# Performance work log

Hardware: AMD Instinct MI355X
Metric: run time of the kernel (lower is better)

## Reference

```python
import jax, jax.numpy as jnp
import numpy as np

N = 100000   # nodes
E = 1600000  # edges per meta-path graph
D_IN = 256
H = 4        # num_heads
F = 32       # out_feats per head
D_HID = H * F  # 128
D_SEM = 128  # semantic attention hidden dim
C = 8        # output classes
NEG_SLOPE = 0.2


def setup_inputs() -> dict:
    key = jax.random.key(0)
    ks = jax.random.split(key, 24)
    inp = {
        "x": jax.random.normal(ks[0], (N, D_IN), dtype=jnp.float32),
        "src0": jax.random.randint(ks[1], (E,), 0, N),
        "dst0": jax.random.randint(ks[2], (E,), 0, N),
        "ew0": jax.random.uniform(ks[3], (E,), dtype=jnp.float32),
        "src1": jax.random.randint(ks[4], (E,), 0, N),
        "dst1": jax.random.randint(ks[5], (E,), 0, N),
        "ew1": jax.random.uniform(ks[6], (E,), dtype=jnp.float32),
    }
    s_in = 1.0 / np.sqrt(D_IN)
    s_f = 1.0 / np.sqrt(F)
    s_h = 1.0 / np.sqrt(D_HID)
    s_s = 1.0 / np.sqrt(D_SEM)
    # GAT params for meta-path 0 and 1 (tuple feat -> separate fc_src/fc_dst)
    inp["Wsrc0"] = jax.random.normal(ks[7], (D_IN, D_HID), dtype=jnp.float32) * s_in
    inp["Wdst0"] = jax.random.normal(ks[8], (D_IN, D_HID), dtype=jnp.float32) * s_in
    inp["al0"] = jax.random.normal(ks[9], (H, F), dtype=jnp.float32) * s_f
    inp["ar0"] = jax.random.normal(ks[10], (H, F), dtype=jnp.float32) * s_f
    inp["b0"] = jnp.zeros((D_HID,), dtype=jnp.float32)
    inp["Wsrc1"] = jax.random.normal(ks[11], (D_IN, D_HID), dtype=jnp.float32) * s_in
    inp["Wdst1"] = jax.random.normal(ks[12], (D_IN, D_HID), dtype=jnp.float32) * s_in
    inp["al1"] = jax.random.normal(ks[13], (H, F), dtype=jnp.float32) * s_f
    inp["ar1"] = jax.random.normal(ks[14], (H, F), dtype=jnp.float32) * s_f
    inp["b1"] = jnp.zeros((D_HID,), dtype=jnp.float32)
    # Semantic attention: Linear(D_HID->128) -> tanh -> Linear(128->1, no bias)
    inp["Wp1"] = jax.random.normal(ks[15], (D_HID, D_SEM), dtype=jnp.float32) * s_h
    inp["bp1"] = jnp.zeros((D_SEM,), dtype=jnp.float32)
    inp["Wp2"] = jax.random.normal(ks[16], (D_SEM, 1), dtype=jnp.float32) * s_s
    # Prediction head
    inp["Wo"] = jax.random.normal(ks[17], (D_HID, C), dtype=jnp.float32) * s_h
    inp["bo"] = jnp.zeros((C,), dtype=jnp.float32)
    return inp


def gat_conv(x, Wsrc, Wdst, al, ar, b, src, dst, ew):
    # feat_src/feat_dst: [N, H, F]
    fs = (x @ Wsrc).reshape(N, H, F)
    fd = (x @ Wdst).reshape(N, H, F)
    el = jnp.einsum('nhf,hf->nh', fs, al)  # [N, H]
    er = jnp.einsum('nhf,hf->nh', fd, ar)  # [N, H]
    e = jax.nn.leaky_relu(el[src] + er[dst], negative_slope=NEG_SLOPE)  # [E, H]
    a = jax.nn.sigmoid(e) * ew[:, None]  # [E, H]  (sigmoid attention * edge_weight)
    m = fs[src] * a[:, :, None]  # [E, H, F]
    out = jax.ops.segment_sum(m, dst, num_segments=N)  # [N, H, F]
    out = out + b.reshape(1, H, F)
    return jax.nn.elu(out).reshape(N, H * F)


def semantic_attention(z, Wp1, bp1, Wp2):
    # z: [N, P, D_HID]
    w = jnp.tanh(z @ Wp1 + bp1) @ Wp2  # [N, P, 1]
    w = w.mean(axis=0)                  # [P, 1]
    beta = jax.nn.softmax(w, axis=0)    # softmax over meta-paths
    return (beta[None] * z).sum(axis=1)  # [N, D_HID]


def reference(x, src0, dst0, ew0, src1, dst1, ew1,
              Wsrc0, Wdst0, al0, ar0, b0,
              Wsrc1, Wdst1, al1, ar1, b1,
              Wp1, bp1, Wp2, Wo, bo):
    z0 = gat_conv(x, Wsrc0, Wdst0, al0, ar0, b0, src0, dst0, ew0)
    z1 = gat_conv(x, Wsrc1, Wdst1, al1, ar1, b1, src1, dst1, ew1)
    z = jnp.stack([z0, z1], axis=1)  # [N, 2, H*F]
    h = semantic_attention(z, Wp1, bp1, Wp2)  # [N, H*F]
    return h @ Wo + bo  # [N, C]
```

## Files before the change

kernel.cpp:

```cpp
#include <hip/hip_runtime.h>
#include <hip/hip_fp16.h>
#include <math.h>

#define N_NODES 100000
#define N_EDGES 1600000
#define D_IN    256
#define D_HID   128
#define NH      4
#define NF      32
#define D_SEM   128
#define NC      8
#define NEG_SLOPE 0.2f
#define BUCKET  64
#define BIN_SHIFT 9
#define BINS    196
#define BIN_CAP 9216
#define CHUNK   8192

typedef _Float16 half8 __attribute__((ext_vector_type(8)));
typedef float    floatx4 __attribute__((ext_vector_type(4)));

struct BinArgs {
    const int*   src[2];
    const int*   dst[2];
    const float* ew[2];
    int*         gcur[2];
    uint2*       binned[2];
};
struct BucketArgs {
    const int*   gcur[2];
    const uint2* binned[2];
    int*         cnt[2];
    unsigned*    edg[2];
};

__global__ __launch_bounds__(256) void prep(const float* __restrict__ Ws0,
                                            const float* __restrict__ Ws1,
                                            const float* __restrict__ Wd0,
                                            const float* __restrict__ ar0,
                                            const float* __restrict__ Wd1,
                                            const float* __restrict__ ar1,
                                            const float* __restrict__ Wp1,
                                            __half* __restrict__ WTA,
                                            __half* __restrict__ WP1T) {
    int g = blockIdx.x * 256 + threadIdx.x;
    if (g < 32768) {
        int col = g >> 8, k = g & 255;
        WTA[(size_t)col*256 + k] = __float2half_rn(Ws0[k*D_HID + col]);
    } else if (g < 65536) {
        int g2 = g - 32768;
        int col = g2 >> 8, k = g2 & 255;
        WTA[(size_t)(128 + col)*256 + k] = __float2half_rn(Ws1[k*D_HID + col]);
    } else if (g < 69632) {
        int g2 = g - 65536;
        int j = g2 >> 8, k = g2 & 255;
        float s = 0.f;
        if (j < 8) {
            int p = j >> 2, h = j & 3;
            const float* Wd = p ? Wd1 : Wd0;
            const float* ar = p ? ar1 : ar0;
            for (int f = 0; f < NF; ++f)
                s = fmaf(Wd[k*D_HID + h*NF + f], ar[h*NF + f], s);
        }
        WTA[(size_t)(256 + j)*256 + k] = __float2half_rn(s);
    } else if (g < 86016) {
        int g2 = g - 69632;
        int c = g2 >> 7, k = g2 & 127;
        WP1T[g2] = __float2half_rn(Wp1[k*D_SEM + c]);
    }
}

__global__ __launch_bounds__(256) void fs_all(const float* __restrict__ x,
                                              const __half* __restrict__ WTA,
                                              const float* __restrict__ al0,
                                              const float* __restrict__ al1,
                                              __half* __restrict__ FS0,
                                              __half* __restrict__ FS1,
                                              float* __restrict__ eler) {
    __shared__ unsigned short xs[64][256];
    __shared__ unsigned short wsB[272][64];
    int tid = threadIdx.x;
    int row0 = blockIdx.x * 64;
    int wid = tid >> 6, lane = tid & 63;
    int lr = lane & 15, lk = lane >> 4;

    #pragma unroll
    for (int i = 0; i < 8; ++i) {
        int id = tid + i*256;
        int r = id >> 5, c8 = (id & 31) << 3;
        int grow = row0 + r;
        float4 v0 = make_float4(0.f,0.f,0.f,0.f), v1 = v0;
        if (grow < N_NODES) {
            v0 = *(const float4*)&x[(size_t)grow*D_IN + c8];
            v1 = *(const float4*)&x[(size_t)grow*D_IN + c8 + 4];
        }
        __half2 h0 = __floats2half2_rn(v0.x, v0.y);
        __half2 h1 = __floats2half2_rn(v0.z, v0.w);
        __half2 h2 = __floats2half2_rn(v1.x, v1.y);
        __half2 h3 = __floats2half2_rn(v1.z, v1.w);
        uint4 pk;
        pk.x = *(unsigned*)&h0; pk.y = *(unsigned*)&h1;
        pk.z = *(unsigned*)&h2; pk.w = *(unsigned*)&h3;
        int ch = c8 >> 3;
        *(uint4*)&xs[r][((ch ^ (r & 7)) << 3)] = pk;
    }

    floatx4 acc[4][4];
    floatx4 acc4[4];
    #pragma unroll
    for (int m = 0; m < 4; ++m) {
        acc4[m] = (floatx4){0.f, 0.f, 0.f, 0.f};
        #pragma unroll
        for (int n = 0; n < 4; ++n) acc[m][n] = (floatx4){0.f, 0.f, 0.f, 0.f};
    }

    for (int kc = 0; kc < 4; ++kc) {
        #pragma unroll
        for (int i = 0; i < 17; ++i) {
            int id = tid + i*256;
            int col = id >> 4, c4 = (id & 15) << 2;
            uint2 pk = *(const uint2*)&WTA[(size_t)col*256 + kc*64 + c4];
            int cc = (((c4 >> 3) ^ (col & 7)) << 3) + (c4 & 7);
            *(uint2*)&wsB[col][cc] = pk;
        }
        __syncthreads();
        #pragma unroll
        for (int kk = 0; kk < 2; ++kk) {
            int kl = kk*4 + lk;
            int kg = kc*8 + kl;
            half8 a[4], b[5];
            #pragma unroll
            for (int m = 0; m < 4; ++m) {
                int r = m*16 + lr;
                a[m] = *(half8*)&xs[r][((kg ^ (r & 7)) << 3)];
            }
            #pragma unroll
            for (int n = 0; n < 4; ++n) {
                int c = wid*64 + n*16 + lr;
                b[n] = *(half8*)&wsB[c][((kl ^ (c & 7)) << 3)];
            }
            if (wid == 0) {
                int c = 256 + lr;
                b[4] = *(half8*)&wsB[c][((kl ^ (c & 7)) << 3)];
            }
            #pragma unroll
            for (int m = 0; m < 4; ++m)
                #pragma unroll
                for (int n = 0; n < 4; ++n)
                    acc[m][n] = __builtin_amdgcn_mfma_f32_16x16x32_f16(a[m], b[n], acc[m][n], 0, 0, 0);
            if (wid == 0) {
                #pragma unroll
                for (int m = 0; m < 4; ++m)
                    acc4[m] = __builtin_amdgcn_mfma_f32_16x16x32_f16(a[m], b[4], acc4[m], 0, 0, 0);
            }
        }
        __syncthreads();
    }

    {
        int p = wid >> 1;
        const float* al = p ? al1 : al0;
        int h0 = (wid & 1) * 2;
        float av00 = al[h0*NF + lr],     av01 = al[h0*NF + 16 + lr];
        float av10 = al[(h0+1)*NF + lr], av11 = al[(h0+1)*NF + 16 + lr];
        #pragma unroll
        for (int m = 0; m < 4; ++m)
            #pragma unroll
            for (int r4 = 0; r4 < 4; ++r4) {
                float s0 = acc[m][0][r4]*av00 + acc[m][1][r4]*av01;
                float s1 = acc[m][2][r4]*av10 + acc[m][3][r4]*av11;
                #pragma unroll
                for (int o = 1; o < 16; o <<= 1) {
                    s0 += __shfl_xor(s0, o);
                    s1 += __shfl_xor(s1, o);
                }
                int row = row0 + m*16 + lk*4 + r4;
                if (lr == 0 && row < N_NODES) {
                    eler[(p*2)*400000 + row*4 + h0]     = s0;
                    eler[(p*2)*400000 + row*4 + h0 + 1] = s1;
                }
            }
    }
    if (wid == 0 && lr < 8) {
        int p = lr >> 2, h = lr & 3;
        #pragma unroll
        for (int m = 0; m < 4; ++m)
            #pragma unroll
            for (int r4 = 0; r4 < 4; ++r4) {
                int row = row0 + m*16 + lk*4 + r4;
                if (row < N_NODES)
                    eler[(p*2+1)*400000 + row*4 + h] = acc4[m][r4];
            }
    }

    __syncthreads();
    #pragma unroll
    for (int n = 0; n < 4; ++n) {
        int col = wid*64 + n*16 + lr;
        #pragma unroll
        for (int m = 0; m < 4; ++m)
            #pragma unroll
            for (int r4 = 0; r4 < 4; ++r4) {
                int rr = m*16 + lk*4 + r4;
                __half hv = __float2half_rn(acc[m][n][r4]);
                xs[rr][col] = *(unsigned short*)&hv;
            }
    }
    __syncthreads();
    #pragma unroll
    for (int i = 0; i < 8; ++i) {
        int id = tid + i*256;
        int r = id >> 5, c8 = (id & 31) << 3;
        int grow = row0 + r;
        if (grow < N_NODES) {
            uint4 pk = *(uint4*)&xs[r][c8];
            if (c8 < 128) *(uint4*)&FS0[(size_t)grow*D_HID + c8]       = pk;
            else          *(uint4*)&FS1[(size_t)grow*D_HID + c8 - 128] = pk;
        }
    }
}

__global__ __launch_bounds__(1024) void bin_kernel(BinArgs A) {
    __shared__ uint2 stage[CHUNK];
    __shared__ unsigned char binof[CHUNK];
    __shared__ int bcnt[256], boff[256], gbase[256], brun[256];
    int P = blockIdx.y;
    const int*   src = A.src[P];
    const int*   dst = A.dst[P];
    const float* ew  = A.ew[P];
    int*         gcur = A.gcur[P];
    uint2*       binned = A.binned[P];

    int tid = threadIdx.x;
    int c0 = blockIdx.x * CHUNK;
    int C = N_EDGES - c0; if (C > CHUNK) C = CHUNK;
    if (C <= 0) return;

    if (tid < 256) bcnt[tid] = 0;
    __syncthreads();
    for (int j = tid; j < C; j += 1024)
        atomicAdd(&bcnt[dst[c0 + j] >> BIN_SHIFT], 1);
    __syncthreads();

    int v = (tid < 256) ? bcnt[tid] : 0;
    if (tid < 256) boff[tid] = v;
    __syncthreads();
    for (int o = 1; o < 256; o <<= 1) {
        int u = (tid < 256 && tid >= o) ? boff[tid - o] : 0;
        __syncthreads();
        if (tid < 256) boff[tid] += u;
        __syncthreads();
    }
    if (tid < 256) {
        boff[tid] -= v;
        brun[tid] = 0;
        if (tid < BINS) gbase[tid] = v ? atomicAdd(&gcur[tid], v) : 0;
    }
    __syncthreads();

    for (int j = tid; j < C; j += 1024) {
        int e = c0 + j;
        int d = dst[e];
        int b = d >> BIN_SHIFT;
        unsigned q = (unsigned)(ew[e] * 32767.f + 0.5f);
        int p = atomicAdd(&brun[b], 1);
        int sl = boff[b] + p;
        stage[sl] = make_uint2(((unsigned)src[e] << 15) | q, (unsigned)d);
        binof[sl] = (unsigned char)b;
    }
    __syncthreads();

    for (int j = tid; j < C; j += 1024) {
        int b = binof[j];
        int off = gbase[b] + (j - boff[b]);
        if (off < BIN_CAP) binned[b * BIN_CAP + off] = stage[j];
    }
}

__global__ __launch_bounds__(1024) void bucket_kernel(BucketArgs A) {
    __shared__ unsigned buck[256 * BUCKET];
    __shared__ int lcnt[256];
    int P = blockIdx.y;
    const int*   gcur   = A.gcur[P];
    const uint2* binned = A.binned[P];
    int*         cnt    = A.cnt[P];
    unsigned*    edg    = A.edg[P];

    int tid = threadIdx.x;
    int nb = blockIdx.x;
    int b  = nb >> 1;
    int n0 = nb << 8;
    int lo = (nb & 1) << 8;
    if (tid < 256) lcnt[tid] = 0;
    __syncthreads();

    int cE = gcur[b]; if (cE > BIN_CAP) cE = BIN_CAP;
    int bn0 = b << BIN_SHIFT;
    for (int j = tid; j < cE; j += 1024) {
        uint2 r = binned[b * BIN_CAP + j];
        int w = ((int)r.y - bn0) - lo;
        if ((unsigned)w < 256u) {
            int p = atomicAdd(&lcnt[w], 1);
            if (p < BUCKET) buck[(w << 6) + p] = r.x;
        }
    }
    __syncthreads();

    const uint4* b4 = (const uint4*)buck;
    uint4* e4 = (uint4*)edg;
    for (int i = tid; i < 256 * BUCKET / 4; i += 1024) {
        int node = n0 + (i >> 4);
        int used = lcnt[i >> 4];
        if (node < N_NODES && ((i & 15) << 2) < used)
            e4[((size_t)node << 4) + (i & 15)] = b4[i];
    }
    if (tid < 256) {
        int node = n0 + tid;
        if (node < N_NODES) cnt[node] = lcnt[tid] < BUCKET ? lcnt[tid] : BUCKET;
    }
}

__global__ __launch_bounds__(256) void agg_kernel(const __half* __restrict__ FS,
                                                  const float* __restrict__ el,
                                                  const float* __restrict__ er,
                                                  const int* __restrict__ cnt,
                                                  const unsigned* __restrict__ edg,
                                                  const float* __restrict__ bias,
                                                  __half* __restrict__ zh) {
    int wv = (blockIdx.x * 256 + threadIdx.x) >> 6;
    int lane = threadIdx.x & 63;
    if (wv >= N_NODES) return;
    int q  = lane >> 4;
    int ql = lane & 15;
    int hh = lane & 3;
    float erh = er[wv*4 + hh];
    int cn = cnt[wv];
    if (cn > BUCKET) cn = BUCKET;
    int beg = wv << 6;
    const __half* fsq = FS + (ql << 3);

    float4 a0 = make_float4(0.f,0.f,0.f,0.f);
    float4 a1 = make_float4(0.f,0.f,0.f,0.f);

    int nIt = (cn + 15) >> 4;
    for (int it = 0; it < nIt; ++it) {
        int jb = it << 4;
        int sl = jb + (lane >> 2);
        int slc = sl < cn ? sl : cn - 1;
        unsigned w = edg[beg + slc];
        int s = (int)(w >> 15);
        float a = (float)(w & 32767u) * (1.f / 32767.f);
        float v = el[s*4 + hh] + erh;
        v = v > 0.f ? v : NEG_SLOPE * v;
        a = a * __builtin_amdgcn_rcpf(1.f + __expf(-v));
        a = sl < cn ? a : 0.f;
        #pragma unroll
        for (int u = 0; u < 4; ++u) {
            int e = (u << 2) + q;
            int su = jb + e;
            int ssrc = __shfl(s, e << 2);
            uint4 raw = make_uint4(0u, 0u, 0u, 0u);
            if (su < cn) raw = *(const uint4*)&fsq[(size_t)ssrc * D_HID];
            float av = __shfl(a, (e << 2) | (ql >> 2));
            float2 f0 = __half22float2(*(__half2*)&raw.x);
            float2 f1 = __half22float2(*(__half2*)&raw.y);
            float2 f2 = __half22float2(*(__half2*)&raw.z);
            float2 f3 = __half22float2(*(__half2*)&raw.w);
            a0.x = fmaf(f0.x, av, a0.x); a0.y = fmaf(f0.y, av, a0.y);
            a0.z = fmaf(f1.x, av, a0.z); a0.w = fmaf(f1.y, av, a0.w);
            a1.x = fmaf(f2.x, av, a1.x); a1.y = fmaf(f2.y, av, a1.y);
            a1.z = fmaf(f3.x, av, a1.z); a1.w = fmaf(f3.y, av, a1.w);
        }
    }

    #pragma unroll
    for (int o = 16; o < 64; o <<= 1) {
        a0.x += __shfl_xor(a0.x, o); a0.y += __shfl_xor(a0.y, o);
        a0.z += __shfl_xor(a0.z, o); a0.w += __shfl_xor(a0.w, o);
        a1.x += __shfl_xor(a1.x, o); a1.y += __shfl_xor(a1.y, o);
        a1.z += __shfl_xor(a1.z, o); a1.w += __shfl_xor(a1.w, o);
    }

    if (q < 2) {
        int c = (ql << 3) + (q << 2);
        float4 r = q ? a1 : a0;
        float4 bv = *(const float4*)&bias[c];
        r.x += bv.x; r.y += bv.y; r.z += bv.z; r.w += bv.w;
        r.x = r.x > 0.f ? r.x : expm1f(r.x);
        r.y = r.y > 0.f ? r.y : expm1f(r.y);
        r.z = r.z > 0.f ? r.z : expm1f(r.z);
        r.w = r.w > 0.f ? r.w : expm1f(r.w);
        __half2 h0 = __floats2half2_rn(r.x, r.y);
        __half2 h1 = __floats2half2_rn(r.z, r.w);
        uint2 pk; pk.x = *(unsigned*)&h0; pk.y = *(unsigned*)&h1;
        *(uint2*)&zh[(size_t)wv*D_HID + c] = pk;
    }
}

__global__ __launch_bounds__(256) void sem_mfma(const __half* __restrict__ zh0,
                                                const __half* __restrict__ zh1,
                                                const __half* __restrict__ WP1T,
                                                const float* __restrict__ bp1,
                                                const float* __restrict__ Wp2,
                                                float* __restrict__ wsum) {
    __shared__ unsigned short zs[64][128];
    __shared__ unsigned short ps[128][128];
    __shared__ float red[4];
    const __half* z = blockIdx.y ? zh1 : zh0;
    int tid = threadIdx.x;
    int row0 = blockIdx.x * 64;
    int wid = tid >> 6, lane = tid & 63;
    int wm = wid >> 1, wn = wid & 1;
    int lr = lane & 15, lk = lane >> 4;

    #pragma unroll
    for (int i = 0; i < 4; ++i) {
        int id = tid + i*256;
        int r = id >> 4, ch = id & 15;
        int grow = row0 + r;
        uint4 pk = make_uint4(0u, 0u, 0u, 0u);
        if (grow < N_NODES) pk = *(const uint4*)&z[(size_t)grow*D_HID + (ch << 3)];
        *(uint4*)&zs[r][((ch ^ (r & 7)) << 3)] = pk;
    }
    #pragma unroll
    for (int i = 0; i < 16; ++i) {
        int id = tid + i*256;
        int c = id >> 5, k4 = (id & 31) << 2;
        uint2 pk = *(const uint2*)&WP1T[c*128 + k4];
        int cc = (((k4 >> 3) ^ (c & 7)) << 3) + (k4 & 7);
        *(uint2*)&ps[c][cc] = pk;
    }
    __syncthreads();

    floatx4 acc[2][4];
    #pragma unroll
    for (int m = 0; m < 2; ++m)
        #pragma unroll
        for (int n = 0; n < 4; ++n) acc[m][n] = (floatx4){0.f, 0.f, 0.f, 0.f};

    #pragma unroll
    for (int kk = 0; kk < 4; ++kk) {
        int ksub = kk*4 + lk;
        half8 a[2], b[4];
        #pragma unroll
        for (int m = 0; m < 2; ++m) {
            int r = wm*32 + m*16 + lr;
            a[m] = *(half8*)&zs[r][((ksub ^ (r & 7)) << 3)];
        }
        #pragma unroll
        for (int n = 0; n < 4; ++n) {
            int c = wn*64 + n*16 + lr;
            b[n] = *(half8*)&ps[c][((ksub ^ (c & 7)) << 3)];
        }
        #pragma unroll
        for (int m = 0; m < 2; ++m)
            #pragma unroll
            for (int n = 0; n < 4; ++n)
                acc[m][n] = __builtin_amdgcn_mfma_f32_16x16x32_f16(a[m], b[n], acc[m][n], 0, 0, 0);
    }

    float s = 0.f;
    #pragma unroll
    for (int m = 0; m < 2; ++m)
        #pragma unroll
        for (int n = 0; n < 4; ++n) {
            int col = wn*64 + n*16 + lr;
            float bp = bp1[col];
            float w2 = Wp2[col];
            #pragma unroll
            for (int r4 = 0; r4 < 4; ++r4) {
                int grow = row0 + wm*32 + m*16 + lk*4 + r4;
                if (grow < N_NODES) {
                    float v = acc[m][n][r4] + bp;
                    float t = 1.f - 2.f / (__expf(2.f*v) + 1.f);
                    s = fmaf(t, w2, s);
                }
            }
        }
    #pragma unroll
    for (int o = 1; o < 64; o <<= 1) s += __shfl_xor(s, o);
    if (lane == 0) red[wid] = s;
    __syncthreads();
    if (tid == 0) atomicAdd(&wsum[blockIdx.y], red[0] + red[1] + red[2] + red[3]);
}

__global__ __launch_bounds__(256) void final_kernel(const __half* __restrict__ zh0,
                                                    const __half* __restrict__ zh1,
                                                    const float* __restrict__ Wo,
                                                    const float* __restrict__ bo,
                                                    const float* __restrict__ wsum,
                                                    float* __restrict__ out) {
    __shared__ float z0s[32][132];
    __shared__ float z1s[32][132];
    __shared__ float wos[128*8];
    __shared__ float bos[8];
    int tid = threadIdx.x;
    int n0 = blockIdx.x * 32;
    #pragma unroll
    for (int i = 0; i < 4; ++i) wos[tid + i*256] = Wo[tid + i*256];
    if (tid < 8) bos[tid] = bo[tid];
    #pragma unroll
    for (int i = 0; i < 2; ++i) {
        int id = tid + i*256;
        int r = id >> 4, c8 = (id & 15) << 3;
        uint4 p0 = *(const uint4*)&zh0[(size_t)(n0 + r)*D_HID + c8];
        uint4 p1 = *(const uint4*)&zh1[(size_t)(n0 + r)*D_HID + c8];
        float2 q0 = __half22float2(*(__half2*)&p0.x);
        float2 q1 = __half22float2(*(__half2*)&p0.y);
        float2 q2 = __half22float2(*(__half2*)&p0.z);
        float2 q3 = __half22float2(*(__half2*)&p0.w);
        *(float4*)&z0s[r][c8]     = make_float4(q0.x, q0.y, q1.x, q1.y);
        *(float4*)&z0s[r][c8 + 4] = make_float4(q2.x, q2.y, q3.x, q3.y);
        q0 = __half22float2(*(__half2*)&p1.x);
        q1 = __half22float2(*(__half2*)&p1.y);
        q2 = __half22float2(*(__half2*)&p1.z);
        q3 = __half22float2(*(__half2*)&p1.w);
        *(float4*)&z1s[r][c8]     = make_float4(q0.x, q0.y, q1.x, q1.y);
        *(float4*)&z1s[r][c8 + 4] = make_float4(q2.x, q2.y, q3.x, q3.y);
    }
    __syncthreads();

    float w0 = wsum[0] * (1.f / N_NODES), w1 = wsum[1] * (1.f / N_NODES);
    float m = fmaxf(w0, w1);
    float e0 = __expf(w0 - m), e1 = __expf(w1 - m);
    float b0 = e0 / (e0 + e1), b1 = 1.f - b0;

    int node = tid >> 3, c = tid & 7;
    float s = bos[c];
    #pragma unroll 8
    for (int k = 0; k < 128; ++k) {
        float hk = b0 * z0s[node][k] + b1 * z1s[node][k];
        s = fmaf(hk, wos[k*8 + c], s);
    }
    out[(n0 + node)*NC + c] = s;
}

extern "C" void kernel_launch(void* const* d_in, const int* in_sizes, int n_in,
                              void* d_out, int out_size, void* d_ws, size_t ws_size,
                              hipStream_t stream) {
    const float* x     = (const float*)d_in[0];
    const int*   src0  = (const int*)  d_in[1];
    const int*   dst0  = (const int*)  d_in[2];
    const float* ew0   = (const float*)d_in[3];
    const int*   src1  = (const int*)  d_in[4];
    const int*   dst1  = (const int*)  d_in[5];
    const float* ew1   = (const float*)d_in[6];
    const float* Wsrc0 = (const float*)d_in[7];
    const float* Wdst0 = (const float*)d_in[8];
    const float* al0   = (const float*)d_in[9];
    const float* ar0   = (const float*)d_in[10];
    const float* b0    = (const float*)d_in[11];
    const float* Wsrc1 = (const float*)d_in[12];
    const float* Wdst1 = (const float*)d_in[13];
    const float* al1   = (const float*)d_in[14];
    const float* ar1   = (const float*)d_in[15];
    const float* b1    = (const float*)d_in[16];
    const float* Wp1   = (const float*)d_in[17];
    const float* bp1   = (const float*)d_in[18];
    const float* Wp2   = (const float*)d_in[19];
    const float* Wo    = (const float*)d_in[20];
    const float* bo    = (const float*)d_in[21];
    float* out = (float*)d_out;

    float*    ws     = (float*)d_ws;
    __half*   FS0    = (__half*)ws;
    __half*   FS1    = (__half*)(ws + 6400000);
    __half*   ZH0    = (__half*)(ws + 12800000);
    __half*   ZH1    = (__half*)(ws + 19200000);
    float*    ELER   = ws + 25600000;
    float*    WSUM   = ELER + 1600000;
    __half*   WTA    = (__half*)(WSUM + 8);
    __half*   WP1T   = (__half*)((float*)WTA + 34816);
    int*      CNT0   = (int*)((float*)WP1T + 8192);
    int*      CNT1   = CNT0  + 100000;
    int*      GCUR0  = CNT1  + 100000;
    int*      GCUR1  = GCUR0 + 256;
    unsigned* EDG0   = (unsigned*)(GCUR1 + 256);
    uint2*    BINNED0= (uint2*)(EDG0 + 6400000);
    float*    endser = (float*)BINNED0 + 2*(size_t)BINS*BIN_CAP;
    unsigned* EDG1   = (unsigned*)endser;
    uint2*    BINNED1= (uint2*)(EDG1 + 6400000);
    size_t fused_bytes = (size_t)((float*)BINNED1 + 2*(size_t)BINS*BIN_CAP - ws) * 4;
    bool fused = ws_size >= fused_bytes;
    if (!fused) { EDG1 = EDG0; BINNED1 = BINNED0; }

    hipMemsetAsync(GCUR0, 0, sizeof(int)*512, stream);
    hipMemsetAsync(WSUM, 0, sizeof(float)*4, stream);

    prep<<<336, 256, 0, stream>>>(Wsrc0, Wsrc1, Wdst0, ar0, Wdst1, ar1, Wp1, WTA, WP1T);
    fs_all<<<(N_NODES + 63)/64, 256, 0, stream>>>(x, WTA, al0, al1, FS0, FS1, ELER);

    int nchunks = (N_EDGES + CHUNK - 1) / CHUNK;
    if (fused) {
        BinArgs ba = {{src0, src1}, {dst0, dst1}, {ew0, ew1},
                      {GCUR0, GCUR1}, {BINNED0, BINNED1}};
        bin_kernel<<<dim3(nchunks, 2), 1024, 0, stream>>>(ba);
        BucketArgs ka = {{GCUR0, GCUR1}, {BINNED0, BINNED1},
                         {CNT0, CNT1}, {EDG0, EDG1}};
        bucket_kernel<<<dim3(2*BINS, 2), 1024, 0, stream>>>(ka);
        agg_kernel<<<(N_NODES*64)/256, 256, 0, stream>>>(FS0, ELER, ELER + 400000, CNT0, EDG0, b0, ZH0);
        agg_kernel<<<(N_NODES*64)/256, 256, 0, stream>>>(FS1, ELER + 800000, ELER + 1200000, CNT1, EDG1, b1, ZH1);
    } else {
        BinArgs ba0 = {{src0, src0}, {dst0, dst0}, {ew0, ew0},
                       {GCUR0, GCUR0}, {BINNED0, BINNED0}};
        BucketArgs ka0 = {{GCUR0, GCUR0}, {BINNED0, BINNED0},
                          {CNT0, CNT0}, {EDG0, EDG0}};
        bin_kernel<<<dim3(nchunks, 1), 1024, 0, stream>>>(ba0);
        bucket_kernel<<<dim3(2*BINS, 1), 1024, 0, stream>>>(ka0);
        agg_kernel<<<(N_NODES*64)/256, 256, 0, stream>>>(FS0, ELER, ELER + 400000, CNT0, EDG0, b0, ZH0);
        BinArgs ba1 = {{src1, src1}, {dst1, dst1}, {ew1, ew1},
                       {GCUR1, GCUR1}, {BINNED0, BINNED0}};
        BucketArgs ka1 = {{GCUR1, GCUR1}, {BINNED0, BINNED0},
                          {CNT1, CNT1}, {EDG0, EDG0}};
        bin_kernel<<<dim3(nchunks, 1), 1024, 0, stream>>>(ba1);
        bucket_kernel<<<dim3(2*BINS, 1), 1024, 0, stream>>>(ka1);
        agg_kernel<<<(N_NODES*64)/256, 256, 0, stream>>>(FS1, ELER + 800000, ELER + 1200000, CNT1, EDG0, b1, ZH1);
    }

    dim3 semgrid((N_NODES + 63)/64, 2);
    sem_mfma<<<semgrid, 256, 0, stream>>>(ZH0, ZH1, WP1T, bp1, Wp2, WSUM);
    final_kernel<<<N_NODES/32, 256, 0, stream>>>(ZH0, ZH1, Wo, bo, WSUM, out);
}
```

Measured before the change: 549.8 us.

## Split node-feature projection kernel across meta-paths via second grid dimension

The fused projection kernel that computed both meta-paths' source features plus attention logits in one block is split so that each block handles a single meta-path (blockIdx.y). The per-wave accumulator count halves, the weight staging buffer shrinks, and the launch bound asks for 4 blocks per CU, all aimed at higher occupancy and more parallel blocks. The cost is that each x tile is loaded and converted to half twice, once per meta-path. The prep kernel's er-weight layout is padded to 16 columns per path to match.

```diff
diff --git a/kernel.cpp b/kernel.cpp
--- a/kernel.cpp
+++ b/kernel.cpp
@@ -51,36 +51,38 @@
         int g2 = g - 32768;
         int col = g2 >> 8, k = g2 & 255;
         WTA[(size_t)(128 + col)*256 + k] = __float2half_rn(Ws1[k*D_HID + col]);
-    } else if (g < 69632) {
+    } else if (g < 73728) {
         int g2 = g - 65536;
         int j = g2 >> 8, k = g2 & 255;
+        int p = j >> 4, hh = j & 15;
         float s = 0.f;
-        if (j < 8) {
-            int p = j >> 2, h = j & 3;
+        if (hh < 4) {
             const float* Wd = p ? Wd1 : Wd0;
             const float* ar = p ? ar1 : ar0;
             for (int f = 0; f < NF; ++f)
-                s = fmaf(Wd[k*D_HID + h*NF + f], ar[h*NF + f], s);
+                s = fmaf(Wd[k*D_HID + hh*NF + f], ar[hh*NF + f], s);
         }
         WTA[(size_t)(256 + j)*256 + k] = __float2half_rn(s);
-    } else if (g < 86016) {
-        int g2 = g - 69632;
+    } else if (g < 90112) {
+        int g2 = g - 73728;
         int c = g2 >> 7, k = g2 & 127;
         WP1T[g2] = __float2half_rn(Wp1[k*D_SEM + c]);
     }
 }
 
-__global__ __launch_bounds__(256) void fs_all(const float* __restrict__ x,
-                                              const __half* __restrict__ WTA,
-                                              const float* __restrict__ al0,
-                                              const float* __restrict__ al1,
-                                              __half* __restrict__ FS0,
-                                              __half* __restrict__ FS1,
-                                              float* __restrict__ eler) {
+__global__ __launch_bounds__(256, 4) void fs_half(const float* __restrict__ x,
+                                                  const __half* __restrict__ WTA,
+                                                  const float* __restrict__ al0,
+                                                  const float* __restrict__ al1,
+                                                  __half* __restrict__ FS0,
+                                                  __half* __restrict__ FS1,
+                                                  float* __restrict__ eler) {
     __shared__ unsigned short xs[64][256];
-    __shared__ unsigned short wsB[272][64];
+    __shared__ unsigned short wsB[144][64];
     int tid = threadIdx.x;
     int row0 = blockIdx.x * 64;
+    int P = blockIdx.y;
+    __half* FSP = P ? FS1 : FS0;
     int wid = tid >> 6, lane = tid & 63;
     int lr = lane & 15, lk = lane >> 4;
 
@@ -105,118 +107,109 @@
         *(uint4*)&xs[r][((ch ^ (r & 7)) << 3)] = pk;
     }
 
-    floatx4 acc[4][4];
+    floatx4 acc[4][2];
     floatx4 acc4[4];
     #pragma unroll
     for (int m = 0; m < 4; ++m) {
         acc4[m] = (floatx4){0.f, 0.f, 0.f, 0.f};
         #pragma unroll
-        for (int n = 0; n < 4; ++n) acc[m][n] = (floatx4){0.f, 0.f, 0.f, 0.f};
-    }
+        for (int n = 0; n < 2; ++n) acc[m][n] = (floatx4){0.f, 0.f, 0.f, 0.f};
+    }
+    __syncthreads();
 
     for (int kc = 0; kc < 4; ++kc) {
         #pragma unroll
-        for (int i = 0; i < 17; ++i) {
+        for (int i = 0; i < 9; ++i) {
             int id = tid + i*256;
-            int col = id >> 4, c4 = (id & 15) << 2;
-            uint2 pk = *(const uint2*)&WTA[(size_t)col*256 + kc*64 + c4];
-            int cc = (((c4 >> 3) ^ (col & 7)) << 3) + (c4 & 7);
-            *(uint2*)&wsB[col][cc] = pk;
+            int cl = id >> 4, c4 = (id & 15) << 2;
+            int gcol = (cl < 128) ? (P*128 + cl) : (256 + P*16 + (cl - 128));
+            uint2 pk = *(const uint2*)&WTA[(size_t)gcol*256 + kc*64 + c4];
+            int cc = (((c4 >> 3) ^ (cl & 7)) << 3) + (c4 & 7);
+            *(uint2*)&wsB[cl][cc] = pk;
         }
         __syncthreads();
         #pragma unroll
         for (int kk = 0; kk < 2; ++kk) {
             int kl = kk*4 + lk;
             int kg = kc*8 + kl;
-            half8 a[4], b[5];
+            half8 a[4], b[2], b4;
+            #pragma unroll
+            for (int n = 0; n < 2; ++n) {
+                int cl = wid*32 + n*16 + lr;
+                b[n] = *(half8*)&wsB[cl][((kl ^ (cl & 7)) << 3)];
+            }
+            if (wid == 0) {
+                int cl = 128 + lr;
+                b4 = *(half8*)&wsB[cl][((kl ^ (cl & 7)) << 3)];
+            }
             #pragma unroll
             for (int m = 0; m < 4; ++m) {
                 int r = m*16 + lr;
                 a[m] = *(half8*)&xs[r][((kg ^ (r & 7)) << 3)];
             }
             #pragma unroll
-            for (int n = 0; n < 4; ++n) {
-                int c = wid*64 + n*16 + lr;
-                b[n] = *(half8*)&wsB[c][((kl ^ (c & 7)) << 3)];
-            }
-            if (wid == 0) {
-                int c = 256 + lr;
-                b[4] = *(half8*)&wsB[c][((kl ^ (c & 7)) << 3)];
-            }
-            #pragma unroll
             for (int m = 0; m < 4; ++m)
                 #pragma unroll
-                for (int n = 0; n < 4; ++n)
+                for (int n = 0; n < 2; ++n)
                     acc[m][n] = __builtin_amdgcn_mfma_f32_16x16x32_f16(a[m], b[n], acc[m][n], 0, 0, 0);
             if (wid == 0) {
                 #pragma unroll
                 for (int m = 0; m < 4; ++m)
-                    acc4[m] = __builtin_amdgcn_mfma_f32_16x16x32_f16(a[m], b[4], acc4[m], 0, 0, 0);
+                    acc4[m] = __builtin_amdgcn_mfma_f32_16x16x32_f16(a[m], b4, acc4[m], 0, 0, 0);
             }
         }
         __syncthreads();
     }
 
     {
-        int p = wid >> 1;
-        const float* al = p ? al1 : al0;
-        int h0 = (wid & 1) * 2;
-        float av00 = al[h0*NF + lr],     av01 = al[h0*NF + 16 + lr];
-        float av10 = al[(h0+1)*NF + lr], av11 = al[(h0+1)*NF + 16 + lr];
+        const float* al = P ? al1 : al0;
+        float av0 = al[wid*NF + lr];
+        float av1 = al[wid*NF + 16 + lr];
         #pragma unroll
         for (int m = 0; m < 4; ++m)
             #pragma unroll
             for (int r4 = 0; r4 < 4; ++r4) {
-                float s0 = acc[m][0][r4]*av00 + acc[m][1][r4]*av01;
-                float s1 = acc[m][2][r4]*av10 + acc[m][3][r4]*av11;
+                float s0 = acc[m][0][r4]*av0 + acc[m][1][r4]*av1;
                 #pragma unroll
-                for (int o = 1; o < 16; o <<= 1) {
-                    s0 += __shfl_xor(s0, o);
-                    s1 += __shfl_xor(s1, o);
-                }
+                for (int o = 1; o < 16; o <<= 1) s0 += __shfl_xor(s0, o);
                 int row = row0 + m*16 + lk*4 + r4;
-                if (lr == 0 && row < N_NODES) {
-                    eler[(p*2)*400000 + row*4 + h0]     = s0;
-                    eler[(p*2)*400000 + row*4 + h0 + 1] = s1;
-                }
-            }
-    }
-    if (wid == 0 && lr < 8) {
-        int p = lr >> 2, h = lr & 3;
+                if (lr == 0 && row < N_NODES)
+                    eler[(P*2)*400000 + row*4 + wid] = s0;
+            }
+    }
+    if (wid == 0 && lr < 4) {
         #pragma unroll
         for (int m = 0; m < 4; ++m)
             #pragma unroll
             for (int r4 = 0; r4 < 4; ++r4) {
                 int row = row0 + m*16 + lk*4 + r4;
                 if (row < N_NODES)
-                    eler[(p*2+1)*400000 + row*4 + h] = acc4[m][r4];
-            }
-    }
-
-    __syncthreads();
-    #pragma unroll
-    for (int n = 0; n < 4; ++n) {
-        int col = wid*64 + n*16 + lr;
+                    eler[(P*2+1)*400000 + row*4 + lr] = acc4[m][r4];
+            }
+    }
+
+    __syncthreads();
+    unsigned short* cstage = &xs[0][0];
+    #pragma unroll
+    for (int n = 0; n < 2; ++n) {
+        int cl = wid*32 + n*16 + lr;
         #pragma unroll
         for (int m = 0; m < 4; ++m)
             #pragma unroll
             for (int r4 = 0; r4 < 4; ++r4) {
                 int rr = m*16 + lk*4 + r4;
                 __half hv = __float2half_rn(acc[m][n][r4]);
-                xs[rr][col] = *(unsigned short*)&hv;
-            }
-    }
-    __syncthreads();
-    #pragma unroll
-    for (int i = 0; i < 8; ++i) {
+                cstage[rr*128 + cl] = *(unsigned short*)&hv;
+            }
+    }
+    __syncthreads();
+    #pragma unroll
+    for (int i = 0; i < 4; ++i) {
         int id = tid + i*256;
-        int r = id >> 5, c8 = (id & 31) << 3;
+        int r = id >> 4, c8 = (id & 15) << 3;
         int grow = row0 + r;
-        if (grow < N_NODES) {
-            uint4 pk = *(uint4*)&xs[r][c8];
-            if (c8 < 128) *(uint4*)&FS0[(size_t)grow*D_HID + c8]       = pk;
-            else          *(uint4*)&FS1[(size_t)grow*D_HID + c8 - 128] = pk;
-        }
+        if (grow < N_NODES)
+            *(uint4*)&FSP[(size_t)grow*D_HID + c8] = *(uint4*)&cstage[r*128 + c8];
     }
 }
 
@@ -570,7 +563,7 @@
     float*    ELER   = ws + 25600000;
     float*    WSUM   = ELER + 1600000;
     __half*   WTA    = (__half*)(WSUM + 8);
-    __half*   WP1T   = (__half*)((float*)WTA + 34816);
+    __half*   WP1T   = (__half*)((float*)WTA + 36864);
     int*      CNT0   = (int*)((float*)WP1T + 8192);
     int*      CNT1   = CNT0  + 100000;
     int*      GCUR0  = CNT1  + 100000;
@@ -587,8 +580,9 @@
     hipMemsetAsync(GCUR0, 0, sizeof(int)*512, stream);
     hipMemsetAsync(WSUM, 0, sizeof(float)*4, stream);
 
-    prep<<<336, 256, 0, stream>>>(Wsrc0, Wsrc1, Wdst0, ar0, Wdst1, ar1, Wp1, WTA, WP1T);
-    fs_all<<<(N_NODES + 63)/64, 256, 0, stream>>>(x, WTA, al0, al1, FS0, FS1, ELER);
+    prep<<<352, 256, 0, stream>>>(Wsrc0, Wsrc1, Wdst0, ar0, Wdst1, ar1, Wp1, WTA, WP1T);
+    dim3 fsgrid((N_NODES + 63)/64, 2);
+    fs_half<<<fsgrid, 256, 0, stream>>>(x, WTA, al0, al1, FS0, FS1, ELER);
 
     int nchunks = (N_EDGES + CHUNK - 1) / CHUNK;
     if (fused) {
```

Result: faster. 521.5 us (-5.1%).
